# Kernel optimization log

Measured on AMD Instinct MI355X. Metric: run time of the kernel, lower is better.

## Reference

```python
import jax, jax.numpy as jnp
import numpy as np

N = 8192      # number of points
C = 128       # in_planes = out_planes = mid_planes
K = 16        # nsample (KNN neighbors, includes self)
S = 8         # share_planes
BN_EPS = 1e-5


def setup_inputs() -> dict:
    key = jax.random.key(0)
    ks = jax.random.split(key, 24)
    rn = lambda k, shape, fan: (jax.random.normal(k, shape, jnp.float32) / np.sqrt(fan))
    inp = {
        "p": jax.random.normal(ks[0], (N, 3), jnp.float32),
        "x": jax.random.normal(ks[1], (N, C), jnp.float32),
        # linear_q / linear_k / linear_v  (stored [in, out])
        "Wq": rn(ks[2], (C, C), C),  "bq": jnp.zeros((C,), jnp.float32),
        "Wk": rn(ks[3], (C, C), C),  "bk": jnp.zeros((C,), jnp.float32),
        "Wv": rn(ks[4], (C, C), C),  "bv": jnp.zeros((C,), jnp.float32),
        # linear_p: Linear(3,3) -> BN(3) -> ReLU -> Linear(3, C)
        "Wp1": rn(ks[5], (3, 3), 3), "bp1": jnp.zeros((3,), jnp.float32),
        "g1": jnp.ones((3,), jnp.float32), "be1": jnp.zeros((3,), jnp.float32),
        "Wp2": rn(ks[6], (3, C), 3), "bp2": jnp.zeros((C,), jnp.float32),
        # linear_w: BN(C) -> ReLU -> Linear(C, C//S) -> BN(C//S) -> ReLU -> Linear(C//S, C//S)
        "g2": jnp.ones((C,), jnp.float32), "be2": jnp.zeros((C,), jnp.float32),
        "Ww1": rn(ks[7], (C, C // S), C), "bw1": jnp.zeros((C // S,), jnp.float32),
        "g3": jnp.ones((C // S,), jnp.float32), "be3": jnp.zeros((C // S,), jnp.float32),
        "Ww2": rn(ks[8], (C // S, C // S), C // S), "bw2": jnp.zeros((C // S,), jnp.float32),
    }
    return inp


def _bn_eval(t, gamma, beta):
    # BatchNorm1d in eval mode with running stats (mean=0, var=1); channel is last axis here.
    return t * (gamma / np.sqrt(1.0 + BN_EPS)) + beta


def reference(p, x, Wq, bq, Wk, bk, Wv, bv, Wp1, bp1, g1, be1, Wp2, bp2,
              g2, be2, Ww1, bw1, g3, be3, Ww2, bw2):
    # ---- queryandgroup: KNN (self-inclusive), relative xyz, gathered features, distances ----
    sq = jnp.sum(p * p, axis=-1)                       # [N]
    d2 = sq[:, None] + sq[None, :] - 2.0 * (p @ p.T)   # [N, N] pairwise squared dist
    neg_d2, idx = jax.lax.top_k(-d2, K)                # [N, K] nearest (self first)
    dist = jnp.sqrt(jnp.maximum(-neg_d2, 0.0))         # [N, K] Euclidean distance
    p_r = p[idx] - p[:, None, :]                       # [N, K, 3] relative position
    x_e = x[idx]                                       # [N, K, C] neighbor features

    # ---- q / k / v projections ----
    x_q = x @ Wq + bq                                  # [N, C]
    x_k = x_e @ Wk + bk                                # [N, K, C]
    x_v = x_e @ Wv + bv                                # [N, K, C]

    # ---- linear_p on relative positions ----
    pr = p_r @ Wp1 + bp1
    pr = jax.nn.relu(_bn_eval(pr, g1, be1))
    pr = pr @ Wp2 + bp2                                # [N, K, C]

    # ---- attention scores: subtractive + relative-pos, then linear_w MLP ----
    w = x_q[:, None, :] - x_k + pr                     # [N, K, C]
    w = jax.nn.relu(_bn_eval(w, g2, be2))
    w = w @ Ww1 + bw1                                  # [N, K, C//S]
    w = jax.nn.relu(_bn_eval(w, g3, be3))
    w = w @ Ww2 + bw2                                  # [N, K, C//S]
    w = jax.nn.softmax(w, axis=1)                      # softmax over neighbors

    # ---- distance-weighted values, grouped weighted sum ----
    dw = jnp.exp(-dist)[..., None]                     # [N, K, 1]
    v = (x_v * dw + pr).reshape(N, K, S, C // S)       # [N, K, S, C//S]
    out = jnp.sum(v * w[:, :, None, :], axis=1).reshape(N, C)
    return out
```

## Files before the change

### kernel.cpp

```cpp
#include <hip/hip_runtime.h>
#include <math.h>

#define NPTS 8192
#define CCH  128
#define KNN  16
#define BN_RS 0.9999950000374997f

typedef unsigned long long u64;
typedef unsigned short u16;
typedef __attribute__((ext_vector_type(8))) short short8;
typedef __attribute__((ext_vector_type(4))) float f32x4;

__device__ __forceinline__ u16 f2bf(float f) {
    unsigned u = __float_as_uint(f);
    u += 0x7FFFu + ((u >> 16) & 1u);
    return (u16)(u >> 16);
}

__device__ __forceinline__ void bf8_to_f(const uint4 u, float* f) {
    f[0] = __uint_as_float(u.x << 16); f[1] = __uint_as_float(u.x & 0xffff0000u);
    f[2] = __uint_as_float(u.y << 16); f[3] = __uint_as_float(u.y & 0xffff0000u);
    f[4] = __uint_as_float(u.z << 16); f[5] = __uint_as_float(u.z & 0xffff0000u);
    f[6] = __uint_as_float(u.w << 16); f[7] = __uint_as_float(u.w & 0xffff0000u);
}

__global__ __launch_bounds__(256) void pack_kernel(const float* __restrict__ p,
                                                   float4* __restrict__ c4,
                                                   const float* __restrict__ Ww1,
                                                   const float* __restrict__ Ww2,
                                                   u16* __restrict__ w1p,
                                                   u16* __restrict__ w2p) {
    const int t = threadIdx.x;
    const int j = blockIdx.x * 256 + t;
    if (j < NPTS) {
        const float x = p[3 * j + 0], y = p[3 * j + 1], z = p[3 * j + 2];
        c4[j] = make_float4(x, y, z, x * x + y * y + z * z);
    }
    if (blockIdx.x == 0) {
        {
            const int lg = t >> 7, rem = t & 127, lr = rem >> 3, e = rem & 7;
            w2p[t] = f2bf(Ww2[((lg * 8 + e) * 16 + lr) & 255]);
        }
        #pragma unroll
        for (int jj = 0; jj < 8; ++jj) {
            const int e2 = t + jj * 256;
            const int m = e2 & 15, c = e2 >> 4;
            const int byte = m * 256 + ((c * 2) ^ ((m & 7) << 4));
            w1p[byte >> 1] = f2bf(Ww1[e2]);
        }
    }
}

#define QPB   8
#define CAP   104
#define TILE  1024
#define SAMPN 4096

__device__ __forceinline__ u64 bitonic64(u64 v, const int lane) {
    #pragma unroll
    for (int k = 2; k <= 64; k <<= 1) {
        #pragma unroll
        for (int j = k >> 1; j > 0; j >>= 1) {
            const u64  o       = __shfl_xor(v, j);
            const bool takemin = (((lane & j) == 0) == ((lane & k) == 0));
            v = ((o < v) == takemin) ? o : v;
        }
    }
    return v;
}

__device__ __forceinline__ float bitonicf(float v, const int lane) {
    #pragma unroll
    for (int k = 2; k <= 64; k <<= 1) {
        #pragma unroll
        for (int j = k >> 1; j > 0; j >>= 1) {
            const float o      = __shfl_xor(v, j);
            const bool takemin = (((lane & j) == 0) == ((lane & k) == 0));
            v = ((o < v) == takemin) ? o : v;
        }
    }
    return v;
}

__device__ __forceinline__ float make_d2(const float4 c, const float m2x, const float m2y,
                                         const float m2z, const float qb) {
    float d2 = fmaf(m2x, c.x, fmaf(m2y, c.y, fmaf(m2z, c.z, c.w + qb)));
    return fmaxf(d2, 0.0f);
}

__global__ __launch_bounds__(256) void knn_kernel(const float4* __restrict__ c4,
                                                  int* __restrict__ oidx,
                                                  float* __restrict__ od2) {
    __shared__ float4 s_pt[TILE];
    __shared__ float  s_min[QPB][256];
    __shared__ float  s_tau[QPB];
    __shared__ u64    s_col[QPB][CAP];
    __shared__ int    s_cnt[QPB];

    const int t     = threadIdx.x;
    const int wave  = t >> 6;
    const int lane  = t & 63;
    const int qbase = blockIdx.x * QPB;

    float m2x[QPB], m2y[QPB], m2z[QPB], qb[QPB];
    #pragma unroll
    for (int qi = 0; qi < QPB; ++qi) {
        const float4 q = c4[qbase + qi];
        m2x[qi] = -2.0f * q.x;
        m2y[qi] = -2.0f * q.y;
        m2z[qi] = -2.0f * q.z;
        qb[qi]  = q.w;
    }
    if (t < QPB) s_cnt[t] = 0;

    float bd[QPB];
    #pragma unroll
    for (int qi = 0; qi < QPB; ++qi) bd[qi] = 3.0e38f;

    const int base = wave * (TILE / 4);
    for (int tb = 0; tb < SAMPN; tb += TILE) {
        __syncthreads();
        #pragma unroll
        for (int jj = 0; jj < 4; ++jj) s_pt[t + jj * 256] = c4[tb + t + jj * 256];
        __syncthreads();
        #pragma unroll
        for (int it = 0; it < 4; ++it) {
            const float4 c = s_pt[base + it * 64 + lane];
            #pragma unroll
            for (int qi = 0; qi < QPB; ++qi)
                bd[qi] = fminf(bd[qi], make_d2(c, m2x[qi], m2y[qi], m2z[qi], qb[qi]));
        }
    }

    #pragma unroll
    for (int qi = 0; qi < QPB; ++qi) s_min[qi][t] = bd[qi];
    __syncthreads();
    #pragma unroll
    for (int u = 0; u < 2; ++u) {
        const int qi = wave * 2 + u;
        float v = fminf(fminf(s_min[qi][lane], s_min[qi][64 + lane]),
                        fminf(s_min[qi][128 + lane], s_min[qi][192 + lane]));
        v = bitonicf(v, lane);
        if (lane == 15) s_tau[qi] = v;
    }
    __syncthreads();
    float tauf[QPB];
    #pragma unroll
    for (int qi = 0; qi < QPB; ++qi) tauf[qi] = s_tau[qi];

    for (int tb = 0; tb < NPTS; tb += TILE) {
        __syncthreads();
        #pragma unroll
        for (int jj = 0; jj < 4; ++jj) s_pt[t + jj * 256] = c4[tb + t + jj * 256];
        __syncthreads();
        #pragma unroll
        for (int it = 0; it < 4; ++it) {
            const int idx = base + it * 64 + lane;
            const float4 c = s_pt[idx];
            const int j = tb + idx;
            #pragma unroll
            for (int qi = 0; qi < QPB; ++qi) {
                const float d = make_d2(c, m2x[qi], m2y[qi], m2z[qi], qb[qi]);
                if (d <= tauf[qi]) {
                    const int pos = atomicAdd(&s_cnt[qi], 1);
                    if (pos < CAP)
                        s_col[qi][pos] = ((u64)__float_as_uint(d) << 32) | (u64)(unsigned)j;
                }
            }
        }
    }
    __syncthreads();

    #pragma unroll 1
    for (int u = 0; u < 2; ++u) {
        const int qi = wave * 2 + u;
        const int q  = qbase + qi;
        int M = s_cnt[qi];

        if (M > CAP) {
            float fb = 3.0e38f;
            for (int l = lane; l < NPTS; l += 64)
                fb = fminf(fb, make_d2(c4[l], m2x[qi], m2y[qi], m2z[qi], qb[qi]));
            const float s    = bitonicf(fb, lane);
            const float tau2 = __shfl(s, 15);
            if (lane == 0) s_cnt[qi] = 0;
            for (int l = lane; l < NPTS; l += 64) {
                const float d = make_d2(c4[l], m2x[qi], m2y[qi], m2z[qi], qb[qi]);
                if (d <= tau2) {
                    const int pos = atomicAdd(&s_cnt[qi], 1);
                    if (pos < CAP)
                        s_col[qi][pos] = ((u64)__float_as_uint(d) << 32) | (u64)(unsigned)l;
                }
            }
            M = s_cnt[qi];
            if (M > CAP) M = CAP;
        }

        if (M <= 64) {
            u64 v = (lane < M) ? s_col[qi][lane] : ~0ull;
            v = bitonic64(v, lane);
            if (lane < KNN) {
                oidx[q * KNN + lane] = (int)(v & 0xffffffffu);
                od2 [q * KNN + lane] = __uint_as_float((unsigned)(v >> 32));
            }
        } else {
            u64 a = (lane < M) ? s_col[qi][lane] : ~0ull;
            a = bitonic64(a, lane);
            u64 b = (lane + 64 < M) ? s_col[qi][lane + 64] : ~0ull;
            b = bitonic64(b, lane);
            const u64 bs = __shfl(b, lane & 15);
            u64 mv = (lane < 16) ? a : ((lane < 32) ? bs : ~0ull);
            mv = bitonic64(mv, lane);
            if (lane < KNN) {
                oidx[q * KNN + lane] = (int)(mv & 0xffffffffu);
                od2 [q * KNN + lane] = __uint_as_float((unsigned)(mv >> 32));
            }
        }
    }
}

__global__ __launch_bounds__(256) void gemm3_kernel(
    const float* __restrict__ x,
    const float* __restrict__ Wq, const float* __restrict__ bq,
    const float* __restrict__ Wk, const float* __restrict__ bk,
    const float* __restrict__ Wv, const float* __restrict__ bv,
    float* __restrict__ xq, u16* __restrict__ xk16, u16* __restrict__ xv16) {
    const int which = blockIdx.z;
    const float* W    = (which == 0) ? Wq : (which == 1) ? Wk : Wv;
    const float* bias = (which == 0) ? bq : (which == 1) ? bk : bv;

    const int row0 = blockIdx.x * 64;
    const int col0 = blockIdx.y * 64;

    __shared__ float AsT[64][65];
    __shared__ float Bs[64][68];

    const int t  = threadIdx.x;
    const int lr = t >> 4;
    const int lc = t & 15;
    const int or0 = (t >> 4) * 4;
    const int oc0 = (t & 15) * 4;

    float acc[4][4] = {};

    for (int kk = 0; kk < CCH; kk += 64) {
        __syncthreads();
        #pragma unroll
        for (int i = 0; i < 4; ++i) {
            const int r = lr + i * 16;
            const float4 av = *(const float4*)&x[(size_t)(row0 + r) * CCH + kk + lc * 4];
            AsT[lc * 4 + 0][r] = av.x;
            AsT[lc * 4 + 1][r] = av.y;
            AsT[lc * 4 + 2][r] = av.z;
            AsT[lc * 4 + 3][r] = av.w;
            *(float4*)&Bs[r][lc * 4] =
                *(const float4*)&W[(size_t)(kk + r) * CCH + col0 + lc * 4];
        }
        __syncthreads();
        #pragma unroll 8
        for (int k = 0; k < 64; ++k) {
            const float4 a = *(const float4*)&AsT[k][or0];
            const float4 b = *(const float4*)&Bs[k][oc0];
            acc[0][0] += a.x * b.x; acc[0][1] += a.x * b.y; acc[0][2] += a.x * b.z; acc[0][3] += a.x * b.w;
            acc[1][0] += a.y * b.x; acc[1][1] += a.y * b.y; acc[1][2] += a.y * b.z; acc[1][3] += a.y * b.w;
            acc[2][0] += a.z * b.x; acc[2][1] += a.z * b.y; acc[2][2] += a.z * b.z; acc[2][3] += a.z * b.w;
            acc[3][0] += a.w * b.x; acc[3][1] += a.w * b.y; acc[3][2] += a.w * b.z; acc[3][3] += a.w * b.w;
        }
    }

    const float4 bb = *(const float4*)&bias[col0 + oc0];
    if (which == 0) {
        #pragma unroll
        for (int i = 0; i < 4; ++i) {
            const int r = row0 + or0 + i;
            float4 o;
            o.x = acc[i][0] + bb.x;
            o.y = acc[i][1] + bb.y;
            o.z = acc[i][2] + bb.z;
            o.w = acc[i][3] + bb.w;
            *(float4*)&xq[(size_t)r * CCH + col0 + oc0] = o;
        }
    } else {
        u16* o16 = (which == 1) ? xk16 : xv16;
        #pragma unroll
        for (int i = 0; i < 4; ++i) {
            const int r = row0 + or0 + i;
            ushort4 h;
            h.x = f2bf(acc[i][0] + bb.x);
            h.y = f2bf(acc[i][1] + bb.y);
            h.z = f2bf(acc[i][2] + bb.z);
            h.w = f2bf(acc[i][3] + bb.w);
            *(ushort4*)&o16[(size_t)r * CCH + col0 + oc0] = h;
        }
    }
}

__global__ __launch_bounds__(256) void fused_kernel(
    const float* __restrict__ p,
    const float* __restrict__ xqg, const u16* __restrict__ xkg, const u16* __restrict__ xvg,
    const int* __restrict__ nidx, const float* __restrict__ nd2,
    const float* __restrict__ Wp1, const float* __restrict__ bp1,
    const float* __restrict__ g1,  const float* __restrict__ be1,
    const float* __restrict__ Wp2, const float* __restrict__ bp2,
    const float* __restrict__ g2,  const float* __restrict__ be2,
    const u16* __restrict__ w1p,   const float* __restrict__ bw1,
    const float* __restrict__ g3,  const float* __restrict__ be3,
    const u16* __restrict__ w2p,   const float* __restrict__ bw2,
    float* __restrict__ out) {
    const int i = blockIdx.x;
    const int t = threadIdx.x;

    __shared__ __align__(16) u16 s_wv[2048];
    __shared__ __align__(16) u16 s_rr[256];
    __shared__ float s_val[16][132];
    __shared__ float s_wnT[16][20];

    const int k  = t >> 4;
    const int tl = t & 15;
    const int c0 = tl * 8;

    const int   jn  = nidx[i * KNN + k];
    const float d2v = nd2[i * KNN + k];
    const uint4 ku = *(const uint4*)&xkg[(size_t)jn * CCH + c0];
    const uint4 vu = *(const uint4*)&xvg[(size_t)jn * CCH + c0];

    const float dw  = __expf(-sqrtf(fmaxf(d2v, 0.f)));
    const float prx = p[jn * 3 + 0] - p[i * 3 + 0];
    const float pry = p[jn * 3 + 1] - p[i * 3 + 1];
    const float prz = p[jn * 3 + 2] - p[i * 3 + 2];
    float tt[3];
    #pragma unroll
    for (int e = 0; e < 3; ++e) {
        float v = prx * Wp1[0 * 3 + e] + pry * Wp1[1 * 3 + e] + prz * Wp1[2 * 3 + e] + bp1[e];
        v = v * (g1[e] * BN_RS) + be1[e];
        tt[e] = fmaxf(v, 0.f);
    }

    float xk8[8], xv8[8];
    bf8_to_f(ku, xk8);
    bf8_to_f(vu, xv8);

    float wv8[8];
    #pragma unroll
    for (int h = 0; h < 2; ++h) {
        const int cc = c0 + h * 4;
        const float4 w0  = *(const float4*)&Wp2[cc];
        const float4 w1  = *(const float4*)&Wp2[128 + cc];
        const float4 w2  = *(const float4*)&Wp2[256 + cc];
        const float4 bp  = *(const float4*)&bp2[cc];
        const float4 xq4 = *(const float4*)&xqg[(size_t)i * CCH + cc];
        const float4 gg  = *(const float4*)&g2[cc];
        const float4 bb  = *(const float4*)&be2[cc];
        float4 val4;
        {
            const float pr = tt[0] * w0.x + tt[1] * w1.x + tt[2] * w2.x + bp.x;
            wv8[h * 4 + 0] = fmaxf(((xq4.x - xk8[h * 4 + 0]) + pr) * (gg.x * BN_RS) + bb.x, 0.f);
            val4.x = xv8[h * 4 + 0] * dw + pr;
        }
        {
            const float pr = tt[0] * w0.y + tt[1] * w1.y + tt[2] * w2.y + bp.y;
            wv8[h * 4 + 1] = fmaxf(((xq4.y - xk8[h * 4 + 1]) + pr) * (gg.y * BN_RS) + bb.y, 0.f);
            val4.y = xv8[h * 4 + 1] * dw + pr;
        }
        {
            const float pr = tt[0] * w0.z + tt[1] * w1.z + tt[2] * w2.z + bp.z;
            wv8[h * 4 + 2] = fmaxf(((xq4.z - xk8[h * 4 + 2]) + pr) * (gg.z * BN_RS) + bb.z, 0.f);
            val4.z = xv8[h * 4 + 2] * dw + pr;
        }
        {
            const float pr = tt[0] * w0.w + tt[1] * w1.w + tt[2] * w2.w + bp.w;
            wv8[h * 4 + 3] = fmaxf(((xq4.w - xk8[h * 4 + 3]) + pr) * (gg.w * BN_RS) + bb.w, 0.f);
            val4.w = xv8[h * 4 + 3] * dw + pr;
        }
        *(float4*)&s_val[k][cc] = val4;
    }

    {
        uint4 wp;
        wp.x = (unsigned)f2bf(wv8[0]) | ((unsigned)f2bf(wv8[1]) << 16);
        wp.y = (unsigned)f2bf(wv8[2]) | ((unsigned)f2bf(wv8[3]) << 16);
        wp.z = (unsigned)f2bf(wv8[4]) | ((unsigned)f2bf(wv8[5]) << 16);
        wp.w = (unsigned)f2bf(wv8[6]) | ((unsigned)f2bf(wv8[7]) << 16);
        const int byte = k * 256 + ((c0 * 2) ^ ((k & 7) << 4));
        *(uint4*)((char*)s_wv + byte) = wp;
    }
    __syncthreads();

    if (t < 64) {
        const int l  = t;
        const int lr = l & 15;
        const int lg = l >> 4;

        f32x4 acc = {0.f, 0.f, 0.f, 0.f};
        #pragma unroll
        for (int c = 0; c < 4; ++c) {
            const int off = ((lg * 16 + 64 * c) ^ ((lr & 7) << 4));
            const short8 a = *(const short8*)((const char*)s_wv + lr * 256 + off);
            const short8 b = *(const short8*)((const char*)w1p  + lr * 256 + off);
            acc = __builtin_amdgcn_mfma_f32_16x16x32_bf16(a, b, acc, 0, 0, 0);
        }
        const float bw1m = bw1[lr];
        const float g3m  = g3[lr] * BN_RS;
        const float be3m = be3[lr];
        #pragma unroll
        for (int r = 0; r < 4; ++r) {
            const float rr = fmaxf((acc[r] + bw1m) * g3m + be3m, 0.f);
            *(u16*)((char*)s_rr + (lg * 4 + r) * 32 + lr * 2) = f2bf(rr);
        }

        short8 a2 = (short8){0, 0, 0, 0, 0, 0, 0, 0};
        short8 b2 = (short8){0, 0, 0, 0, 0, 0, 0, 0};
        if (lg < 2) {
            a2 = *(const short8*)((const char*)s_rr + lr * 32 + lg * 16);
            b2 = *(const short8*)((const char*)w2p + (lg * 16 + lr) * 16);
        }
        f32x4 acc2 = {0.f, 0.f, 0.f, 0.f};
        acc2 = __builtin_amdgcn_mfma_f32_16x16x32_bf16(a2, b2, acc2, 0, 0, 0);

        const float bw2m = bw2[lr];
        float w2v[4];
        #pragma unroll
        for (int r = 0; r < 4; ++r) w2v[r] = acc2[r] + bw2m;

        float mx = fmaxf(fmaxf(w2v[0], w2v[1]), fmaxf(w2v[2], w2v[3]));
        mx = fmaxf(mx, __shfl_xor(mx, 16));
        mx = fmaxf(mx, __shfl_xor(mx, 32));
        float ev[4], ss = 0.f;
        #pragma unroll
        for (int r = 0; r < 4; ++r) { ev[r] = __expf(w2v[r] - mx); ss += ev[r]; }
        ss += __shfl_xor(ss, 16);
        ss += __shfl_xor(ss, 32);
        const float inv = __fdividef(1.f, ss);
        #pragma unroll
        for (int r = 0; r < 4; ++r) s_wnT[lr][lg * 4 + r] = ev[r] * inv;
    }
    __syncthreads();

    if (t < 128) {
        const int c = t, mc = t & 15;
        const float4 wn0 = *(const float4*)&s_wnT[mc][0];
        const float4 wn1 = *(const float4*)&s_wnT[mc][4];
        const float4 wn2 = *(const float4*)&s_wnT[mc][8];
        const float4 wn3 = *(const float4*)&s_wnT[mc][12];
        float o = 0.f;
        o += s_val[0][c]  * wn0.x; o += s_val[1][c]  * wn0.y;
        o += s_val[2][c]  * wn0.z; o += s_val[3][c]  * wn0.w;
        o += s_val[4][c]  * wn1.x; o += s_val[5][c]  * wn1.y;
        o += s_val[6][c]  * wn1.z; o += s_val[7][c]  * wn1.w;
        o += s_val[8][c]  * wn2.x; o += s_val[9][c]  * wn2.y;
        o += s_val[10][c] * wn2.z; o += s_val[11][c] * wn2.w;
        o += s_val[12][c] * wn3.x; o += s_val[13][c] * wn3.y;
        o += s_val[14][c] * wn3.z; o += s_val[15][c] * wn3.w;
        out[(size_t)i * CCH + c] = o;
    }
}

extern "C" void kernel_launch(void* const* d_in, const int* in_sizes, int n_in,
                              void* d_out, int out_size, void* d_ws, size_t ws_size,
                              hipStream_t stream) {
    (void)in_sizes; (void)n_in; (void)out_size; (void)ws_size;
    const float* p   = (const float*)d_in[0];
    const float* x   = (const float*)d_in[1];
    const float* Wq  = (const float*)d_in[2];
    const float* bq  = (const float*)d_in[3];
    const float* Wk  = (const float*)d_in[4];
    const float* bk  = (const float*)d_in[5];
    const float* Wv  = (const float*)d_in[6];
    const float* bv  = (const float*)d_in[7];
    const float* Wp1 = (const float*)d_in[8];
    const float* bp1 = (const float*)d_in[9];
    const float* g1  = (const float*)d_in[10];
    const float* be1 = (const float*)d_in[11];
    const float* Wp2 = (const float*)d_in[12];
    const float* bp2 = (const float*)d_in[13];
    const float* g2  = (const float*)d_in[14];
    const float* be2 = (const float*)d_in[15];
    const float* Ww1 = (const float*)d_in[16];
    const float* bw1 = (const float*)d_in[17];
    const float* g3  = (const float*)d_in[18];
    const float* be3 = (const float*)d_in[19];
    const float* Ww2 = (const float*)d_in[20];
    const float* bw2 = (const float*)d_in[21];
    float* out = (float*)d_out;

    char* ws = (char*)d_ws;
    int*    idxb  = (int*)ws;
    float*  d2b   = (float*)(ws + (size_t)512 * 1024);
    float*  xqb   = (float*)(ws + (size_t)1 * 1024 * 1024);
    u16*    xkb16 = (u16*)(ws + (size_t)5 * 1024 * 1024);
    u16*    xvb16 = (u16*)(ws + (size_t)7 * 1024 * 1024);
    float4* c4b   = (float4*)(ws + (size_t)9 * 1024 * 1024);
    u16*    w1p   = (u16*)(ws + (size_t)9 * 1024 * 1024 + 128 * 1024);
    u16*    w2p   = (u16*)(ws + (size_t)9 * 1024 * 1024 + 132 * 1024);

    pack_kernel<<<dim3(NPTS / 256), dim3(256), 0, stream>>>(p, c4b, Ww1, Ww2, w1p, w2p);
    knn_kernel<<<dim3(NPTS / QPB), dim3(256), 0, stream>>>(c4b, idxb, d2b);
    gemm3_kernel<<<dim3(NPTS / 64, CCH / 64, 3), dim3(256), 0, stream>>>(
        x, Wq, bq, Wk, bk, Wv, bv, xqb, xkb16, xvb16);
    fused_kernel<<<dim3(NPTS), dim3(256), 0, stream>>>(
        p, xqb, xkb16, xvb16, idxb, d2b,
        Wp1, bp1, g1, be1, Wp2, bp2, g2, be2, w1p, bw1, g3, be3, w2p, bw2, out);
}
```

Measured before the change: 85.76 us.

## Use bf16 MFMA for QKV projection with prepacked weights; shrink KNN sample

Replaces the fp32 shared-memory tiled QKV GEMM with bf16 MFMA 16x16x32. Wq, Wk and Wv are prepacked into MFMA fragment layout by extra blocks in pack_kernel, and activations are loaded directly into registers. The KNN sample size for threshold estimation is halved, and the distance is computed with explicit fmas and clamped at zero. The q projection now goes through bf16, which loses precision, and a smaller sample may yield a looser threshold and more overflow fallbacks.

```diff
diff --git a/kernel.cpp b/kernel.cpp
--- a/kernel.cpp
+++ b/kernel.cpp
@@ -24,12 +24,25 @@
     f[6] = __uint_as_float(u.w << 16); f[7] = __uint_as_float(u.w & 0xffff0000u);
 }
 
+__device__ __forceinline__ short8 pack8(const float4 a, const float4 b) {
+    short8 s;
+    s[0] = (short)f2bf(a.x); s[1] = (short)f2bf(a.y);
+    s[2] = (short)f2bf(a.z); s[3] = (short)f2bf(a.w);
+    s[4] = (short)f2bf(b.x); s[5] = (short)f2bf(b.y);
+    s[6] = (short)f2bf(b.z); s[7] = (short)f2bf(b.w);
+    return s;
+}
+
 __global__ __launch_bounds__(256) void pack_kernel(const float* __restrict__ p,
                                                    float4* __restrict__ c4,
                                                    const float* __restrict__ Ww1,
                                                    const float* __restrict__ Ww2,
+                                                   const float* __restrict__ Wq,
+                                                   const float* __restrict__ Wk,
+                                                   const float* __restrict__ Wv,
                                                    u16* __restrict__ w1p,
-                                                   u16* __restrict__ w2p) {
+                                                   u16* __restrict__ w2p,
+                                                   u16* __restrict__ wpack) {
     const int t = threadIdx.x;
     const int j = blockIdx.x * 256 + t;
     if (j < NPTS) {
@@ -48,13 +61,29 @@
             const int byte = m * 256 + ((c * 2) ^ ((m & 7) << 4));
             w1p[byte >> 1] = f2bf(Ww1[e2]);
         }
+    } else if (blockIdx.x <= 24) {
+        const int g0 = (blockIdx.x - 1) * 2048;
+        #pragma unroll
+        for (int jj = 0; jj < 8; ++jj) {
+            const int g   = g0 + t + jj * 256;
+            const int m   = g >> 14;
+            const int u   = g & 16383;
+            const int e   = u & 7;
+            const int l   = (u >> 3) & 63;
+            const int kc  = (u >> 9) & 3;
+            const int ccg = (u >> 11) & 7;
+            const int k   = kc * 32 + ((l >> 4) << 3) + e;
+            const int col = ccg * 16 + (l & 15);
+            const float* W = (m == 0) ? Wq : (m == 1) ? Wk : Wv;
+            wpack[g] = f2bf(W[k * CCH + col]);
+        }
     }
 }
 
 #define QPB   8
 #define CAP   104
 #define TILE  1024
-#define SAMPN 4096
+#define SAMPN 2048
 
 __device__ __forceinline__ u64 bitonic64(u64 v, const int lane) {
     #pragma unroll
@@ -160,11 +189,14 @@
             const int j = tb + idx;
             #pragma unroll
             for (int qi = 0; qi < QPB; ++qi) {
-                const float d = make_d2(c, m2x[qi], m2y[qi], m2z[qi], qb[qi]);
+                const float d = fmaf(m2x[qi], c.x,
+                                 fmaf(m2y[qi], c.y,
+                                  fmaf(m2z[qi], c.z, c.w + qb[qi])));
                 if (d <= tauf[qi]) {
                     const int pos = atomicAdd(&s_cnt[qi], 1);
                     if (pos < CAP)
-                        s_col[qi][pos] = ((u64)__float_as_uint(d) << 32) | (u64)(unsigned)j;
+                        s_col[qi][pos] = ((u64)__float_as_uint(fmaxf(d, 0.f)) << 32)
+                                       | (u64)(unsigned)j;
                 }
             }
         }
@@ -221,76 +253,55 @@
 
 __global__ __launch_bounds__(256) void gemm3_kernel(
     const float* __restrict__ x,
-    const float* __restrict__ Wq, const float* __restrict__ bq,
-    const float* __restrict__ Wk, const float* __restrict__ bk,
-    const float* __restrict__ Wv, const float* __restrict__ bv,
+    const float* __restrict__ bq, const float* __restrict__ bk,
+    const float* __restrict__ bv, const u16* __restrict__ wpack,
     float* __restrict__ xq, u16* __restrict__ xk16, u16* __restrict__ xv16) {
     const int which = blockIdx.z;
-    const float* W    = (which == 0) ? Wq : (which == 1) ? Wk : Wv;
     const float* bias = (which == 0) ? bq : (which == 1) ? bk : bv;
 
-    const int row0 = blockIdx.x * 64;
+    const int t    = threadIdx.x;
+    const int wave = t >> 6;
+    const int l    = t & 63;
+    const int lr   = l & 15;
+    const int lg   = l >> 4;
+
+    const int row0 = blockIdx.x * 64 + wave * 16;
     const int col0 = blockIdx.y * 64;
 
-    __shared__ float AsT[64][65];
-    __shared__ float Bs[64][68];
-
-    const int t  = threadIdx.x;
-    const int lr = t >> 4;
-    const int lc = t & 15;
-    const int or0 = (t >> 4) * 4;
-    const int oc0 = (t & 15) * 4;
-
-    float acc[4][4] = {};
-
-    for (int kk = 0; kk < CCH; kk += 64) {
-        __syncthreads();
-        #pragma unroll
-        for (int i = 0; i < 4; ++i) {
-            const int r = lr + i * 16;
-            const float4 av = *(const float4*)&x[(size_t)(row0 + r) * CCH + kk + lc * 4];
-            AsT[lc * 4 + 0][r] = av.x;
-            AsT[lc * 4 + 1][r] = av.y;
-            AsT[lc * 4 + 2][r] = av.z;
-            AsT[lc * 4 + 3][r] = av.w;
-            *(float4*)&Bs[r][lc * 4] =
-                *(const float4*)&W[(size_t)(kk + r) * CCH + col0 + lc * 4];
-        }
-        __syncthreads();
-        #pragma unroll 8
-        for (int k = 0; k < 64; ++k) {
-            const float4 a = *(const float4*)&AsT[k][or0];
-            const float4 b = *(const float4*)&Bs[k][oc0];
-            acc[0][0] += a.x * b.x; acc[0][1] += a.x * b.y; acc[0][2] += a.x * b.z; acc[0][3] += a.x * b.w;
-            acc[1][0] += a.y * b.x; acc[1][1] += a.y * b.y; acc[1][2] += a.y * b.z; acc[1][3] += a.y * b.w;
-            acc[2][0] += a.z * b.x; acc[2][1] += a.z * b.y; acc[2][2] += a.z * b.z; acc[2][3] += a.z * b.w;
-            acc[3][0] += a.w * b.x; acc[3][1] += a.w * b.y; acc[3][2] += a.w * b.z; acc[3][3] += a.w * b.w;
-        }
-    }
-
-    const float4 bb = *(const float4*)&bias[col0 + oc0];
-    if (which == 0) {
-        #pragma unroll
-        for (int i = 0; i < 4; ++i) {
-            const int r = row0 + or0 + i;
-            float4 o;
-            o.x = acc[i][0] + bb.x;
-            o.y = acc[i][1] + bb.y;
-            o.z = acc[i][2] + bb.z;
-            o.w = acc[i][3] + bb.w;
-            *(float4*)&xq[(size_t)r * CCH + col0 + oc0] = o;
-        }
-    } else {
-        u16* o16 = (which == 1) ? xk16 : xv16;
-        #pragma unroll
-        for (int i = 0; i < 4; ++i) {
-            const int r = row0 + or0 + i;
-            ushort4 h;
-            h.x = f2bf(acc[i][0] + bb.x);
-            h.y = f2bf(acc[i][1] + bb.y);
-            h.z = f2bf(acc[i][2] + bb.z);
-            h.w = f2bf(acc[i][3] + bb.w);
-            *(ushort4*)&o16[(size_t)r * CCH + col0 + oc0] = h;
+    short8 afr[4];
+    #pragma unroll
+    for (int kc = 0; kc < 4; ++kc) {
+        const float4 a0 = *(const float4*)&x[(size_t)(row0 + lr) * CCH + kc * 32 + lg * 8];
+        const float4 a1 = *(const float4*)&x[(size_t)(row0 + lr) * CCH + kc * 32 + lg * 8 + 4];
+        afr[kc] = pack8(a0, a1);
+    }
+
+    f32x4 acc[4] = {{0.f,0.f,0.f,0.f},{0.f,0.f,0.f,0.f},
+                    {0.f,0.f,0.f,0.f},{0.f,0.f,0.f,0.f}};
+    const u16* wp = wpack + which * 16384;
+    #pragma unroll
+    for (int cc = 0; cc < 4; ++cc) {
+        const int ccg = (col0 >> 4) + cc;
+        #pragma unroll
+        for (int kc = 0; kc < 4; ++kc) {
+            const short8 b = *(const short8*)&wp[((ccg * 4 + kc) * 64 + l) * 8];
+            acc[cc] = __builtin_amdgcn_mfma_f32_16x16x32_bf16(afr[kc], b, acc[cc], 0, 0, 0);
+        }
+    }
+
+    #pragma unroll
+    for (int cc = 0; cc < 4; ++cc) {
+        const int col = col0 + cc * 16 + lr;
+        const float bb = bias[col];
+        if (which == 0) {
+            #pragma unroll
+            for (int r = 0; r < 4; ++r)
+                xq[(size_t)(row0 + lg * 4 + r) * CCH + col] = acc[cc][r] + bb;
+        } else {
+            u16* o16 = (which == 1) ? xk16 : xv16;
+            #pragma unroll
+            for (int r = 0; r < 4; ++r)
+                o16[(size_t)(row0 + lg * 4 + r) * CCH + col] = f2bf(acc[cc][r] + bb);
         }
     }
 }
@@ -492,11 +503,13 @@
     float4* c4b   = (float4*)(ws + (size_t)9 * 1024 * 1024);
     u16*    w1p   = (u16*)(ws + (size_t)9 * 1024 * 1024 + 128 * 1024);
     u16*    w2p   = (u16*)(ws + (size_t)9 * 1024 * 1024 + 132 * 1024);
-
-    pack_kernel<<<dim3(NPTS / 256), dim3(256), 0, stream>>>(p, c4b, Ww1, Ww2, w1p, w2p);
+    u16*    wpack = (u16*)(ws + (size_t)9 * 1024 * 1024 + 136 * 1024);
+
+    pack_kernel<<<dim3(NPTS / 256), dim3(256), 0, stream>>>(
+        p, c4b, Ww1, Ww2, Wq, Wk, Wv, w1p, w2p, wpack);
     knn_kernel<<<dim3(NPTS / QPB), dim3(256), 0, stream>>>(c4b, idxb, d2b);
     gemm3_kernel<<<dim3(NPTS / 64, CCH / 64, 3), dim3(256), 0, stream>>>(
-        x, Wq, bq, Wk, bk, Wv, bv, xqb, xkb16, xvb16);
+        x, bq, bk, bv, wpack, xqb, xkb16, xvb16);
     fused_kernel<<<dim3(NPTS), dim3(256), 0, stream>>>(
         p, xqb, xkb16, xvb16, idxb, d2b,
         Wp1, bp1, g1, be1, Wp2, bp2, g2, be2, w1p, bw1, g3, be3, w2p, bw2, out);
```

After: 140.2 us. 63.5% more time.
